# Kernel tuning notes

Measured on AMD Instinct MI355X. Metric: run time of the kernel, lower is better.

## Reference

```python
import jax, jax.numpy as jnp
import numpy as np

IN_F = 4096
OUT_F = 4096
PACKED_IN = IN_F // 16  # 16 ternary values per int32 (2 bits each)
TOKENS = 8192


def _pack(vals_int32):
    # vals_int32: [out, packed_in, 16] with entries in {0,1,2}
    shifts = (jnp.arange(16, dtype=jnp.int32) * 2)
    return jnp.sum(vals_int32 << shifts, axis=-1).astype(jnp.int32)


def _unpack_weight(packed, scale, in_features):
    # packed: [out, packed_in] int32 -> fp32 weight [out, in_features]
    shifts = (jnp.arange(16, dtype=jnp.int32) * 2)
    vals = (packed[:, :, None] >> shifts) & 3           # [out, packed_in, 16]
    w = vals.reshape(packed.shape[0], -1)[:, :in_features]
    return (w.astype(jnp.float32) - 1.0) * scale


def setup_inputs() -> dict:
    key = jax.random.key(0)
    k1, k2 = jax.random.split(key)
    x = jax.random.normal(k1, (TOKENS, IN_F), dtype=jnp.float32)
    # mapped ternary values in {0,1,2} (i.e. w_ternary + 1), packed 2-bit
    mapped = jax.random.randint(k2, (OUT_F, PACKED_IN, 16), 0, 3, dtype=jnp.int32)
    packed_weight = _pack(mapped)
    scale = jnp.float32(0.02)
    return {"x": x, "packed_weight": packed_weight, "scale": scale}


def reference(x, packed_weight, scale):
    # dequantize ternary weight
    w = _unpack_weight(packed_weight, scale, IN_F)      # [out, in]
    # abs-max activation scaling along the last dim
    x_scale = jnp.clip(jnp.max(jnp.abs(x), axis=-1, keepdims=True), 1e-5, None)
    x_scaled = x / x_scale
    out = jnp.einsum('ti,oi->to', x_scaled, w)          # F.linear (no bias)
    return out * x_scale
```

## Files before the change

### kernel.cpp

```cpp
#include <hip/hip_runtime.h>
#include <math.h>

typedef __attribute__((ext_vector_type(4)))  int   i32x4;
typedef __attribute__((ext_vector_type(16))) int   i32x16;
typedef __attribute__((ext_vector_type(4)))  float f32x4;

namespace {
constexpr int IN_F   = 4096;
constexpr int OUT_F  = 4096;
constexpr int TOKENS = 8192;
constexpr int PACKED = IN_F / 16;

constexpr int BM   = 256;
constexpr int BN   = 128;
constexpr int BK   = 64;
constexpr int NTHR = 256;
constexpr int NT   = IN_F / BK;

constexpr size_t XQ_BYTES = (size_t)TOKENS * IN_F;
constexpr size_t XS_BYTES = (size_t)TOKENS * 4;
constexpr size_t BQ_OFF   = XQ_BYTES + XS_BYTES;
constexpr size_t BQ_BYTES = (size_t)PACKED * OUT_F * 16;
constexpr size_t WS_NEED  = BQ_OFF + BQ_BYTES;
}

__device__ __forceinline__ i32x4 unpack16(unsigned w) {
  i32x4 r;
#pragma unroll
  for (int g = 0; g < 4; ++g) {
    unsigned t = (w >> (8 * g)) & 0xFFu;
    unsigned s = (t | (t << 6) | (t << 12) | (t << 18)) & 0x03030303u;
    r[g] = (int)((((s | 0x80808080u) - 0x01010101u) ^ 0x80808080u));
  }
  return r;
}

__global__ __launch_bounds__(256)
void rowquant(const float* __restrict__ X, signed char* __restrict__ XQ,
              float* __restrict__ XS) {
  const int row  = blockIdx.x * 4 + (threadIdx.x >> 6);
  const int lane = threadIdx.x & 63;
  const float* xr = X + (size_t)row * IN_F;

  f32x4 v[16];
  float m = 0.f;
#pragma unroll
  for (int c = 0; c < 16; ++c) {
    v[c] = *(const f32x4*)(xr + c * 256 + lane * 4);
    m = fmaxf(m, fmaxf(fmaxf(fabsf(v[c].x), fabsf(v[c].y)),
                       fmaxf(fabsf(v[c].z), fabsf(v[c].w))));
  }
#pragma unroll
  for (int off = 32; off; off >>= 1) m = fmaxf(m, __shfl_xor(m, off, 64));
  m = fmaxf(m, 1e-5f);
  const float r = 127.f / m;

#pragma unroll
  for (int c = 0; c < 16; ++c) {
    int q0 = (int)rintf(v[c].x * r);
    int q1 = (int)rintf(v[c].y * r);
    int q2 = (int)rintf(v[c].z * r);
    int q3 = (int)rintf(v[c].w * r);
    unsigned d = (q0 & 255) | ((q1 & 255) << 8) | ((q2 & 255) << 16) | ((q3 & 255) << 24);
    *(unsigned*)(XQ + (size_t)row * IN_F + c * 256 + lane * 4) = d;
  }
  if (lane == 0) XS[row] = m;
}

__global__ __launch_bounds__(256)
void unpackB(const unsigned* __restrict__ PW, signed char* __restrict__ BQ) {
  const int g = blockIdx.x * 256 + threadIdx.x;
  const int c = g >> 12;
  const int n = g & 4095;
  i32x4 u = unpack16(PW[(size_t)n * PACKED + c]);
  *(i32x4*)(BQ + ((size_t)c * OUT_F + n) * 16) = u;
}


#define STAGE_A(BUF_, KT_)                                                      \
  {                                                                             \
    _Pragma("unroll")                                                           \
    for (int rb = 0; rb < 4; ++rb) {                                            \
      const signed char* src =                                                  \
          XQ + (size_t)(m0 + rb * 64 + lane) * IN_F + (KT_) * BK + w * 16;      \
      signed char* dst = lA + (BUF_) * 16384 + w * 4096 + rb * 1024;            \
      __builtin_amdgcn_global_load_lds(                                         \
          (const __attribute__((address_space(1))) void*)src,                   \
          (__attribute__((address_space(3))) void*)dst, 16, 0, 0);              \
    }                                                                           \
  }

#define LOAD_B(B_, KT_)                                                         \
  {                                                                             \
    _Pragma("unroll")                                                           \
    for (int nf = 0; nf < 2; ++nf) {                                            \
      _Pragma("unroll")                                                         \
      for (int ks = 0; ks < 2; ++ks)                                            \
        B_[nf][ks] = *(const i32x4*)(BQ +                                       \
            ((size_t)((KT_) * 4 + ks * 2 + h) * OUT_F + nrow[nf]) * 16);        \
      }                                                                         \
  }

#define COMPUTE(BUF_, B_)                                                       \
  {                                                                             \
    _Pragma("unroll")                                                           \
    for (int ks = 0; ks < 2; ++ks) {                                            \
      i32x4 afr[4];                                                             \
      _Pragma("unroll")                                                         \
      for (int mf = 0; mf < 4; ++mf)                                            \
        afr[mf] = *(const i32x4*)(lA + (BUF_) * 16384 + (ks * 2 + h) * 4096 +   \
                                  (wm * 128 + mf * 32 + l31) * 16);             \
      __builtin_amdgcn_s_setprio(1);                                            \
      _Pragma("unroll")                                                         \
      for (int mf = 0; mf < 4; ++mf) {                                          \
        acc[mf][0] = __builtin_amdgcn_mfma_i32_32x32x32_i8(afr[mf], B_[0][ks],  \
                                                           acc[mf][0], 0, 0, 0);\
        acc[mf][1] = __builtin_amdgcn_mfma_i32_32x32x32_i8(afr[mf], B_[1][ks],  \
                                                           acc[mf][1], 0, 0, 0);\
      }                                                                         \
      __builtin_amdgcn_s_setprio(0);                                            \
    }                                                                           \
  }

#define BODY(KT_, BUFC_, BUFS_, BC_, BL_, DOB_, DOA_, VM_)                      \
  {                                                                             \
    if (DOB_) LOAD_B(BL_, (KT_) + 1);                                           \
    if (DOA_) STAGE_A(BUFS_, (KT_) + 2);                                        \
    asm volatile("s_waitcnt vmcnt(" #VM_ ")" ::: "memory");                     \
    __builtin_amdgcn_s_barrier();                                               \
    asm volatile("" ::: "memory");                                              \
    COMPUTE(BUFC_, BC_);                                                        \
  }

__global__ __launch_bounds__(NTHR, 2)
void gemm_i8(const signed char* __restrict__ XQ, const signed char* __restrict__ BQ,
             const float* __restrict__ XS, const float* __restrict__ SC,
             float* __restrict__ OUT) {
  __shared__ signed char lA[4 * 16384];

  const int tid  = threadIdx.x;
  const int lane = tid & 63;
  const int w    = tid >> 6;
  const int wm   = w >> 1;
  const int wn   = w & 1;
  const int l31  = lane & 31;
  const int h    = lane >> 5;

  const int orig = blockIdx.y * gridDim.x + blockIdx.x;
  const int xcd  = orig & 7;
  const int idx  = orig >> 3;
  const int m0   = (idx >> 2) * BM;
  const int n0   = (xcd * 4 + (idx & 3)) * BN;

  const int nrow[2] = { n0 + wn * 64 + 0 * 32 + l31,
                        n0 + wn * 64 + 1 * 32 + l31 };

  i32x16 acc[4][2];
#pragma unroll
  for (int mf = 0; mf < 4; ++mf)
#pragma unroll
    for (int nf = 0; nf < 2; ++nf)
      acc[mf][nf] = (i32x16)(0);

  i32x4 Ba[2][2], Bb[2][2];

  LOAD_B(Ba, 0);
  STAGE_A(0, 0);
  STAGE_A(1, 1);

  for (int kt0 = 0; kt0 < NT - 4; kt0 += 4) {
    BODY(kt0 + 0, 0, 2, Ba, Bb, true, true, 12);
    BODY(kt0 + 1, 1, 3, Bb, Ba, true, true, 12);
    BODY(kt0 + 2, 2, 0, Ba, Bb, true, true, 12);
    BODY(kt0 + 3, 3, 1, Bb, Ba, true, true, 12);
  }
  BODY(NT - 4, 0, 2, Ba, Bb, true,  true,  12);
  BODY(NT - 3, 1, 3, Bb, Ba, true,  true,  12);
  BODY(NT - 2, 2, 0, Ba, Bb, true,  false, 8);
  BODY(NT - 1, 3, 0, Bb, Ba, false, false, 0);

  const float sc = SC[0] / 127.f;
#pragma unroll
  for (int mf = 0; mf < 4; ++mf) {
    float fs[16];
#pragma unroll
    for (int r = 0; r < 16; ++r) {
      const int mm = m0 + wm * 128 + mf * 32 + 4 * h + (r & 3) + 8 * (r >> 2);
      fs[r] = sc * XS[mm];
    }
#pragma unroll
    for (int nf = 0; nf < 2; ++nf) {
      const int ncol = n0 + wn * 64 + nf * 32 + l31;
#pragma unroll
      for (int r = 0; r < 16; ++r) {
        const int mm = m0 + wm * 128 + mf * 32 + 4 * h + (r & 3) + 8 * (r >> 2);
        OUT[(size_t)mm * OUT_F + ncol] = (float)acc[mf][nf][r] * fs[r];
      }
    }
  }
}

__global__ __launch_bounds__(256, 2)
void gemm_i8_pw(const signed char* __restrict__ XQ, const unsigned* __restrict__ PW,
                const float* __restrict__ XS, const float* __restrict__ SC,
                float* __restrict__ OUT) {
  __shared__ signed char lA[256 * 128];

  const int tid  = threadIdx.x;
  const int lane = tid & 63;
  const int w    = tid >> 6;
  const int wm   = w >> 1;
  const int wn   = w & 1;
  const int l31  = lane & 31;
  const int h    = lane >> 5;

  const int m0 = blockIdx.y * 256;
  const int n0 = blockIdx.x * 128;

  i32x16 acc[4][2];
#pragma unroll
  for (int mf = 0; mf < 4; ++mf)
#pragma unroll
    for (int nf = 0; nf < 2; ++nf)
      acc[mf][nf] = (i32x16)(0);

  const unsigned* pb0 = PW + (size_t)(n0 + wn * 64 + 0 * 32 + l31) * PACKED;
  const unsigned* pb1 = PW + (size_t)(n0 + wn * 64 + 1 * 32 + l31) * PACKED;

  for (int kt = 0; kt < IN_F / 128; ++kt) {
#pragma unroll
    for (int cc = 0; cc < 2; ++cc) {
      const int c = w * 2 + cc;
#pragma unroll
      for (int rb = 0; rb < 4; ++rb) {
        const signed char* src =
            XQ + (size_t)(m0 + rb * 64 + lane) * IN_F + kt * 128 + c * 16;
        signed char* dst = lA + c * 4096 + rb * 1024;
        __builtin_amdgcn_global_load_lds(
            (const __attribute__((address_space(1))) void*)src,
            (__attribute__((address_space(3))) void*)dst, 16, 0, 0);
      }
    }

    unsigned bw0[4], bw1[4];
#pragma unroll
    for (int ks = 0; ks < 4; ++ks) {
      bw0[ks] = pb0[kt * 8 + ks * 2 + h];
      bw1[ks] = pb1[kt * 8 + ks * 2 + h];
    }

    __syncthreads();

#pragma unroll
    for (int ks = 0; ks < 4; ++ks) {
      i32x4 bfr0 = unpack16(bw0[ks]);
      i32x4 bfr1 = unpack16(bw1[ks]);
      i32x4 afr[4];
#pragma unroll
      for (int mf = 0; mf < 4; ++mf)
        afr[mf] = *(const i32x4*)(lA + (ks * 2 + h) * 4096 +
                                  (wm * 128 + mf * 32 + l31) * 16);
#pragma unroll
      for (int mf = 0; mf < 4; ++mf) {
        acc[mf][0] = __builtin_amdgcn_mfma_i32_32x32x32_i8(afr[mf], bfr0, acc[mf][0], 0, 0, 0);
        acc[mf][1] = __builtin_amdgcn_mfma_i32_32x32x32_i8(afr[mf], bfr1, acc[mf][1], 0, 0, 0);
      }
    }
    __syncthreads();
  }

  const float sc = SC[0] / 127.f;
#pragma unroll
  for (int mf = 0; mf < 4; ++mf) {
    float fs[16];
#pragma unroll
    for (int r = 0; r < 16; ++r) {
      const int mm = m0 + wm * 128 + mf * 32 + 4 * h + (r & 3) + 8 * (r >> 2);
      fs[r] = sc * XS[mm];
    }
#pragma unroll
    for (int nf = 0; nf < 2; ++nf) {
      const int ncol = n0 + wn * 64 + nf * 32 + l31;
#pragma unroll
      for (int r = 0; r < 16; ++r) {
        const int mm = m0 + wm * 128 + mf * 32 + 4 * h + (r & 3) + 8 * (r >> 2);
        OUT[(size_t)mm * OUT_F + ncol] = (float)acc[mf][nf][r] * fs[r];
      }
    }
  }
}

extern "C" void kernel_launch(void* const* d_in, const int* in_sizes, int n_in,
                              void* d_out, int out_size, void* d_ws, size_t ws_size,
                              hipStream_t stream) {
  const float*    x  = (const float*)d_in[0];
  const unsigned* pw = (const unsigned*)d_in[1];
  const float*    sc = (const float*)d_in[2];
  float*          out = (float*)d_out;

  signed char* xq = (signed char*)d_ws;
  float*       xs = (float*)((char*)d_ws + XQ_BYTES);

  rowquant<<<dim3(TOKENS / 4), dim3(256), 0, stream>>>(x, xq, xs);

  if (ws_size >= WS_NEED) {
    signed char* bq = (signed char*)d_ws + BQ_OFF;
    unpackB<<<dim3(OUT_F * PACKED / 256), dim3(256), 0, stream>>>(pw, bq);
    dim3 grid(OUT_F / BN, TOKENS / BM);
    gemm_i8<<<grid, dim3(NTHR), 0, stream>>>(xq, bq, xs, sc, out);
  } else {
    dim3 grid(OUT_F / 128, TOKENS / 256);
    gemm_i8_pw<<<grid, dim3(256), 0, stream>>>(xq, pw, xs, sc, out);
  }
}
```

Before: 426.8 us.

## Enlarge GEMM tile to 256x256 with LDS-staged B and fuse prep kernels

The int8 GEMM grows from a 256x128 tile with 4 waves to a 256x256 tile with 8 waves and BK=128. B fragments are now staged through LDS with async global-to-LDS loads instead of being read per-wave straight into registers. The pipeline is simplified to double buffering with one full vmcnt(0) wait and barrier per K tile. Row quantisation and weight unpacking are merged into one launch to save a kernel launch. The larger tile raises reuse of A and B per block, but the 128KB of LDS and the full wait per tile may cut occupancy and overlap.

```diff
diff --git a/kernel.cpp b/kernel.cpp
--- a/kernel.cpp
+++ b/kernel.cpp
@@ -12,9 +12,9 @@
 constexpr int PACKED = IN_F / 16;
 
 constexpr int BM   = 256;
-constexpr int BN   = 128;
-constexpr int BK   = 64;
-constexpr int NTHR = 256;
+constexpr int BN   = 256;
+constexpr int BK   = 128;
+constexpr int NTHR = 512;
 constexpr int NT   = IN_F / BK;
 
 constexpr size_t XQ_BYTES = (size_t)TOKENS * IN_F;
@@ -36,44 +36,44 @@
 }
 
 __global__ __launch_bounds__(256)
-void rowquant(const float* __restrict__ X, signed char* __restrict__ XQ,
-              float* __restrict__ XS) {
-  const int row  = blockIdx.x * 4 + (threadIdx.x >> 6);
-  const int lane = threadIdx.x & 63;
-  const float* xr = X + (size_t)row * IN_F;
-
-  f32x4 v[16];
-  float m = 0.f;
-#pragma unroll
-  for (int c = 0; c < 16; ++c) {
-    v[c] = *(const f32x4*)(xr + c * 256 + lane * 4);
-    m = fmaxf(m, fmaxf(fmaxf(fabsf(v[c].x), fabsf(v[c].y)),
-                       fmaxf(fabsf(v[c].z), fabsf(v[c].w))));
-  }
-#pragma unroll
-  for (int off = 32; off; off >>= 1) m = fmaxf(m, __shfl_xor(m, off, 64));
-  m = fmaxf(m, 1e-5f);
-  const float r = 127.f / m;
-
-#pragma unroll
-  for (int c = 0; c < 16; ++c) {
-    int q0 = (int)rintf(v[c].x * r);
-    int q1 = (int)rintf(v[c].y * r);
-    int q2 = (int)rintf(v[c].z * r);
-    int q3 = (int)rintf(v[c].w * r);
-    unsigned d = (q0 & 255) | ((q1 & 255) << 8) | ((q2 & 255) << 16) | ((q3 & 255) << 24);
-    *(unsigned*)(XQ + (size_t)row * IN_F + c * 256 + lane * 4) = d;
-  }
-  if (lane == 0) XS[row] = m;
-}
-
-__global__ __launch_bounds__(256)
-void unpackB(const unsigned* __restrict__ PW, signed char* __restrict__ BQ) {
-  const int g = blockIdx.x * 256 + threadIdx.x;
-  const int c = g >> 12;
-  const int n = g & 4095;
-  i32x4 u = unpack16(PW[(size_t)n * PACKED + c]);
-  *(i32x4*)(BQ + ((size_t)c * OUT_F + n) * 16) = u;
+void prep(const float* __restrict__ X, signed char* __restrict__ XQ,
+          float* __restrict__ XS, const unsigned* __restrict__ PW,
+          signed char* __restrict__ BQ) {
+  if (blockIdx.x < TOKENS / 4) {
+    const int row  = blockIdx.x * 4 + (threadIdx.x >> 6);
+    const int lane = threadIdx.x & 63;
+    const float* xr = X + (size_t)row * IN_F;
+
+    f32x4 v[16];
+    float m = 0.f;
+#pragma unroll
+    for (int c = 0; c < 16; ++c) {
+      v[c] = *(const f32x4*)(xr + c * 256 + lane * 4);
+      m = fmaxf(m, fmaxf(fmaxf(fabsf(v[c].x), fabsf(v[c].y)),
+                         fmaxf(fabsf(v[c].z), fabsf(v[c].w))));
+    }
+#pragma unroll
+    for (int off = 32; off; off >>= 1) m = fmaxf(m, __shfl_xor(m, off, 64));
+    m = fmaxf(m, 1e-5f);
+    const float r = 127.f / m;
+
+#pragma unroll
+    for (int c = 0; c < 16; ++c) {
+      int q0 = (int)rintf(v[c].x * r);
+      int q1 = (int)rintf(v[c].y * r);
+      int q2 = (int)rintf(v[c].z * r);
+      int q3 = (int)rintf(v[c].w * r);
+      unsigned d = (q0 & 255) | ((q1 & 255) << 8) | ((q2 & 255) << 16) | ((q3 & 255) << 24);
+      *(unsigned*)(XQ + (size_t)row * IN_F + c * 256 + lane * 4) = d;
+    }
+    if (lane == 0) XS[row] = m;
+  } else {
+    const int g = (blockIdx.x - TOKENS / 4) * 256 + threadIdx.x;
+    const int c = g >> 12;
+    const int n = g & 4095;
+    i32x4 u = unpack16(PW[(size_t)n * PACKED + c]);
+    *(i32x4*)(BQ + ((size_t)c * OUT_F + n) * 16) = u;
+  }
 }
 
 
@@ -83,77 +83,80 @@
     for (int rb = 0; rb < 4; ++rb) {                                            \
       const signed char* src =                                                  \
           XQ + (size_t)(m0 + rb * 64 + lane) * IN_F + (KT_) * BK + w * 16;      \
-      signed char* dst = lA + (BUF_) * 16384 + w * 4096 + rb * 1024;            \
+      signed char* dst = lA + (BUF_) * 32768 + w * 4096 + rb * 1024;            \
       __builtin_amdgcn_global_load_lds(                                         \
           (const __attribute__((address_space(1))) void*)src,                   \
           (__attribute__((address_space(3))) void*)dst, 16, 0, 0);              \
     }                                                                           \
   }
 
-#define LOAD_B(B_, KT_)                                                         \
+#define STAGE_B(BUF_, KT_)                                                      \
   {                                                                             \
     _Pragma("unroll")                                                           \
-    for (int nf = 0; nf < 2; ++nf) {                                            \
-      _Pragma("unroll")                                                         \
-      for (int ks = 0; ks < 2; ++ks)                                            \
-        B_[nf][ks] = *(const i32x4*)(BQ +                                       \
-            ((size_t)((KT_) * 4 + ks * 2 + h) * OUT_F + nrow[nf]) * 16);        \
-      }                                                                         \
-  }
-
-#define COMPUTE(BUF_, B_)                                                       \
+    for (int j = 0; j < 4; ++j) {                                               \
+      const signed char* src =                                                  \
+          BQ + ((size_t)((KT_) * 8 + w) * OUT_F + n0 + j * 64 + lane) * 16;     \
+      signed char* dst = lB + (BUF_) * 32768 + w * 4096 + j * 1024;             \
+      __builtin_amdgcn_global_load_lds(                                         \
+          (const __attribute__((address_space(1))) void*)src,                   \
+          (__attribute__((address_space(3))) void*)dst, 16, 0, 0);              \
+    }                                                                           \
+  }
+
+#define PHASE(KS_, BUF_)                                                        \
   {                                                                             \
-    _Pragma("unroll")                                                           \
-    for (int ks = 0; ks < 2; ++ks) {                                            \
-      i32x4 afr[4];                                                             \
-      _Pragma("unroll")                                                         \
-      for (int mf = 0; mf < 4; ++mf)                                            \
-        afr[mf] = *(const i32x4*)(lA + (BUF_) * 16384 + (ks * 2 + h) * 4096 +   \
-                                  (wm * 128 + mf * 32 + l31) * 16);             \
-      __builtin_amdgcn_s_setprio(1);                                            \
-      _Pragma("unroll")                                                         \
-      for (int mf = 0; mf < 4; ++mf) {                                          \
-        acc[mf][0] = __builtin_amdgcn_mfma_i32_32x32x32_i8(afr[mf], B_[0][ks],  \
-                                                           acc[mf][0], 0, 0, 0);\
-        acc[mf][1] = __builtin_amdgcn_mfma_i32_32x32x32_i8(afr[mf], B_[1][ks],  \
-                                                           acc[mf][1], 0, 0, 0);\
-      }                                                                         \
-      __builtin_amdgcn_s_setprio(0);                                            \
+    i32x4 afr[4], bfr[2];                                                       \
+    _Pragma("unroll")                                                           \
+    for (int mf = 0; mf < 4; ++mf)                                              \
+      afr[mf] = *(const i32x4*)(lA + (BUF_) * 32768 + ((KS_) * 2 + h) * 4096 +  \
+                                (wm * 128 + mf * 32 + l31) * 16);               \
+    _Pragma("unroll")                                                           \
+    for (int nf = 0; nf < 2; ++nf)                                              \
+      bfr[nf] = *(const i32x4*)(lB + (BUF_) * 32768 + ((KS_) * 2 + h) * 4096 +  \
+                                (wn * 64 + nf * 32 + l31) * 16);                \
+    __builtin_amdgcn_s_setprio(1);                                              \
+    _Pragma("unroll")                                                           \
+    for (int mf = 0; mf < 4; ++mf) {                                            \
+      acc[mf][0] = __builtin_amdgcn_mfma_i32_32x32x32_i8(afr[mf], bfr[0],       \
+                                                         acc[mf][0], 0, 0, 0);  \
+      acc[mf][1] = __builtin_amdgcn_mfma_i32_32x32x32_i8(afr[mf], bfr[1],       \
+                                                         acc[mf][1], 0, 0, 0);  \
     }                                                                           \
-  }
-
-#define BODY(KT_, BUFC_, BUFS_, BC_, BL_, DOB_, DOA_, VM_)                      \
+    __builtin_amdgcn_s_setprio(0);                                              \
+  }
+
+#define TILE(KT_, CUR_, NXT_, PF_)                                              \
   {                                                                             \
-    if (DOB_) LOAD_B(BL_, (KT_) + 1);                                           \
-    if (DOA_) STAGE_A(BUFS_, (KT_) + 2);                                        \
-    asm volatile("s_waitcnt vmcnt(" #VM_ ")" ::: "memory");                     \
+    if (PF_) STAGE_A(NXT_, (KT_) + 1);                                          \
+    PHASE(0, CUR_)                                                              \
+    if (PF_) STAGE_B(NXT_, (KT_) + 1);                                          \
+    PHASE(1, CUR_)                                                              \
+    PHASE(2, CUR_)                                                              \
+    PHASE(3, CUR_)                                                              \
+    asm volatile("s_waitcnt vmcnt(0)" ::: "memory");                            \
     __builtin_amdgcn_s_barrier();                                               \
-    asm volatile("" ::: "memory");                                              \
-    COMPUTE(BUFC_, BC_);                                                        \
   }
 
 __global__ __launch_bounds__(NTHR, 2)
 void gemm_i8(const signed char* __restrict__ XQ, const signed char* __restrict__ BQ,
              const float* __restrict__ XS, const float* __restrict__ SC,
              float* __restrict__ OUT) {
-  __shared__ signed char lA[4 * 16384];
+  __shared__ signed char lA[2 * 32768];
+  __shared__ signed char lB[2 * 32768];
 
   const int tid  = threadIdx.x;
   const int lane = tid & 63;
   const int w    = tid >> 6;
-  const int wm   = w >> 1;
-  const int wn   = w & 1;
+  const int wm   = w >> 2;
+  const int wn   = w & 3;
   const int l31  = lane & 31;
   const int h    = lane >> 5;
 
   const int orig = blockIdx.y * gridDim.x + blockIdx.x;
   const int xcd  = orig & 7;
   const int idx  = orig >> 3;
-  const int m0   = (idx >> 2) * BM;
-  const int n0   = (xcd * 4 + (idx & 3)) * BN;
-
-  const int nrow[2] = { n0 + wn * 64 + 0 * 32 + l31,
-                        n0 + wn * 64 + 1 * 32 + l31 };
+  const int m0   = (idx >> 1) * BM;
+  const int n0   = (xcd * 2 + (idx & 1)) * BN;
 
   i32x16 acc[4][2];
 #pragma unroll
@@ -162,22 +165,17 @@
     for (int nf = 0; nf < 2; ++nf)
       acc[mf][nf] = (i32x16)(0);
 
-  i32x4 Ba[2][2], Bb[2][2];
-
-  LOAD_B(Ba, 0);
   STAGE_A(0, 0);
-  STAGE_A(1, 1);
-
-  for (int kt0 = 0; kt0 < NT - 4; kt0 += 4) {
-    BODY(kt0 + 0, 0, 2, Ba, Bb, true, true, 12);
-    BODY(kt0 + 1, 1, 3, Bb, Ba, true, true, 12);
-    BODY(kt0 + 2, 2, 0, Ba, Bb, true, true, 12);
-    BODY(kt0 + 3, 3, 1, Bb, Ba, true, true, 12);
-  }
-  BODY(NT - 4, 0, 2, Ba, Bb, true,  true,  12);
-  BODY(NT - 3, 1, 3, Bb, Ba, true,  true,  12);
-  BODY(NT - 2, 2, 0, Ba, Bb, true,  false, 8);
-  BODY(NT - 1, 3, 0, Bb, Ba, false, false, 0);
+  STAGE_B(0, 0);
+  asm volatile("s_waitcnt vmcnt(0)" ::: "memory");
+  __builtin_amdgcn_s_barrier();
+
+  for (int kt = 0; kt < NT - 2; kt += 2) {
+    TILE(kt,     0, 1, true);
+    TILE(kt + 1, 1, 0, true);
+  }
+  TILE(NT - 2, 0, 1, true);
+  TILE(NT - 1, 1, 0, false);
 
   const float sc = SC[0] / 127.f;
 #pragma unroll
@@ -301,14 +299,14 @@
   signed char* xq = (signed char*)d_ws;
   float*       xs = (float*)((char*)d_ws + XQ_BYTES);
 
-  rowquant<<<dim3(TOKENS / 4), dim3(256), 0, stream>>>(x, xq, xs);
-
   if (ws_size >= WS_NEED) {
     signed char* bq = (signed char*)d_ws + BQ_OFF;
-    unpackB<<<dim3(OUT_F * PACKED / 256), dim3(256), 0, stream>>>(pw, bq);
+    prep<<<dim3(TOKENS / 4 + OUT_F * PACKED / 256), dim3(256), 0, stream>>>(
+        x, xq, xs, pw, bq);
     dim3 grid(OUT_F / BN, TOKENS / BM);
     gemm_i8<<<grid, dim3(NTHR), 0, stream>>>(xq, bq, xs, sc, out);
   } else {
+    prep<<<dim3(TOKENS / 4), dim3(256), 0, stream>>>(x, xq, xs, pw, nullptr);
     dim3 grid(OUT_F / 128, TOKENS / 256);
     gemm_i8_pw<<<grid, dim3(256), 0, stream>>>(xq, pw, xs, sc, out);
   }
```

Result: faster. 397.0 us (-7.0%).
